# Optimization experiments

Measured on AMD Instinct MI355X. Metric: run time of the kernel, lower is better.

Reference implementation:

```python
import jax, jax.numpy as jnp
import numpy as np

B, T, D, K = 8, 4096, 512, 4096


def setup_inputs() -> dict:
    key = jax.random.key(0)
    k1, k2 = jax.random.split(key)
    x = jax.random.normal(k1, (B, T, D), dtype=jnp.float32)
    embed = jax.random.normal(k2, (K, D), dtype=jnp.float32)
    return {"x": x, "embed": embed}


def reference(x, embed):
    # F.normalize(x, p=2, dim=-1) with eps clamp like torch (eps=1e-12)
    norm = jnp.sqrt(jnp.sum(x * x, axis=-1, keepdims=True))
    xn = x / jnp.maximum(norm, 1e-12)

    flat = xn.reshape(-1, D)  # [(B*T), D]
    x_sq = jnp.sum(flat * flat, axis=1, keepdims=True)           # [(B*T), 1]
    e_sq = jnp.sum(embed * embed, axis=1)[None, :]               # [1, K]
    dist = -(x_sq - 2.0 * (flat @ embed.T) + e_sq)               # [(B*T), K]
    embed_ind = jnp.argmax(dist, axis=-1).reshape(B, T)          # [B, T]

    # decode: embedding gather then 'b n d -> b d n'
    quantize = embed[embed_ind]                                  # [B, T, D]
    quantize = jnp.transpose(quantize, (0, 2, 1))                # [B, D, T]
    return embed_ind, quantize
```

## Files before the change

### kernel.cpp

```cpp
#include <hip/hip_runtime.h>
#include <math.h>

#define BB 8
#define TT 4096
#define DDIM 512
#define KK 4096
#define NN (BB*TT)
#define EPS 0.035f
#define LCAP 2048

typedef __attribute__((ext_vector_type(8))) short bf16x8;
typedef __attribute__((ext_vector_type(4))) float f32x4;

__device__ __forceinline__ void async16(void* lds, const void* g) {
  __builtin_amdgcn_global_load_lds((const __attribute__((address_space(1))) void*)g,
                                   (__attribute__((address_space(3))) void*)lds, 16, 0, 0);
}

__device__ __forceinline__ unsigned pk_bf16(float a, float b) {
  unsigned ua = __float_as_uint(a); ua += 0x7FFFu + ((ua >> 16) & 1u);
  unsigned ub = __float_as_uint(b); ub += 0x7FFFu + ((ub >> 16) & 1u);
  return (ua >> 16) | (ub & 0xFFFF0000u);
}

__global__ __launch_bounds__(256) void prep_kernel(const float* __restrict__ x,
                                                   const float* __restrict__ embed,
                                                   short* __restrict__ xb,
                                                   short* __restrict__ eb,
                                                   float* __restrict__ inv2,
                                                   float* __restrict__ esq) {
  const float* src; short* dst; float* outv; int r; int mode;
  if (blockIdx.x < KK / 4) {
    src = embed; dst = eb; outv = esq; mode = 0;
    r = blockIdx.x * 4 + (threadIdx.x >> 6);
  } else {
    src = x; dst = xb; outv = inv2; mode = 1;
    r = (blockIdx.x - KK / 4) * 4 + (threadIdx.x >> 6);
  }
  int lane = threadIdx.x & 63;
  const float4* row4 = (const float4*)(src + (size_t)r * DDIM);
  float4 v0 = row4[lane];
  float4 v1 = row4[lane + 64];
  uint2 p0, p1;
  p0.x = pk_bf16(v0.x, v0.y); p0.y = pk_bf16(v0.z, v0.w);
  p1.x = pk_bf16(v1.x, v1.y); p1.y = pk_bf16(v1.z, v1.w);
  *(uint2*)(dst + (size_t)r * DDIM + lane * 4) = p0;
  *(uint2*)(dst + (size_t)r * DDIM + 256 + lane * 4) = p1;
  float ss = v0.x*v0.x + v0.y*v0.y + v0.z*v0.z + v0.w*v0.w
           + v1.x*v1.x + v1.y*v1.y + v1.z*v1.z + v1.w*v1.w;
  #pragma unroll
  for (int off = 32; off; off >>= 1) ss += __shfl_down(ss, off);
  if (lane == 0) outv[r] = mode ? 2.0f / fmaxf(sqrtf(ss), 1e-12f) : ss;
}

__global__ __launch_bounds__(256, 2) void vq_mfma(const short* __restrict__ xb,
                                                  const short* __restrict__ eb,
                                                  const float* __restrict__ esq,
                                                  const float* __restrict__ inv2,
                                                  float* __restrict__ cts1,
                                                  float* __restrict__ cts2,
                                                  int* __restrict__ cti) {
  __shared__ short As[128 * 64];
  __shared__ short Bs[128 * 64];
  __shared__ float rS1[2][128];
  __shared__ float rS2[2][128];
  __shared__ int   rI1[2][128];

  const int tid = threadIdx.x;
  const int lane = tid & 63;
  const int w = tid >> 6;
  const int wr = w >> 1, wc = w & 1;
  const int q = lane >> 4, c16 = lane & 15;

  const int mb = blockIdx.x & 255;
  const int kq = blockIdx.x >> 8;
  const int n0 = mb * 128;
  const int kbase = kq * 1024;

  const int srow = w * 32 + (lane >> 3);
  const int scol = ((lane & 7) ^ (lane >> 3)) * 8;
  const short* gA = xb + (size_t)(n0 + srow) * DDIM + scol;

  f32x4 inv4[4];
  #pragma unroll
  for (int ti = 0; ti < 4; ++ti)
    inv4[ti] = *(const f32x4*)&inv2[n0 + wr * 64 + ti * 16 + q * 4];

  for (int p = 0; p < 4; ++p) {
    float cs1[16], cs2[16];
    int   ci1[16];
    #pragma unroll
    for (int s = 0; s < 16; ++s) { cs1[s] = -3e38f; cs2[s] = -3e38f; ci1[s] = 0; }

    for (int cc = 0; cc < 2; ++cc) {
      const int c = p * 2 + cc;
      const int k0c = kbase + c * 128;
      const short* gB = eb + (size_t)(k0c + srow) * DDIM + scol;
      f32x4 acc[4][4];
      #pragma unroll
      for (int ti = 0; ti < 4; ++ti)
        #pragma unroll
        for (int tj = 0; tj < 4; ++tj) acc[ti][tj] = (f32x4){0.f, 0.f, 0.f, 0.f};

      for (int d0 = 0; d0 < DDIM; d0 += 64) {
        #pragma unroll
        for (int i = 0; i < 4; ++i) {
          async16(As + (w * 32 + i * 8) * 64, gA + (size_t)i * 8 * DDIM + d0);
          async16(Bs + (w * 32 + i * 8) * 64, gB + (size_t)i * 8 * DDIM + d0);
        }
        __syncthreads();
        #pragma unroll
        for (int ks = 0; ks < 2; ++ks) {
          const int ko = (((ks << 2) | q) ^ (lane & 7)) << 3;
          bf16x8 af[4], bf[4];
          #pragma unroll
          for (int ti = 0; ti < 4; ++ti)
            af[ti] = *(const bf16x8*)&As[(wr * 64 + ti * 16 + c16) * 64 + ko];
          #pragma unroll
          for (int tj = 0; tj < 4; ++tj)
            bf[tj] = *(const bf16x8*)&Bs[(wc * 64 + tj * 16 + c16) * 64 + ko];
          #pragma unroll
          for (int ti = 0; ti < 4; ++ti)
            #pragma unroll
            for (int tj = 0; tj < 4; ++tj)
              acc[ti][tj] = __builtin_amdgcn_mfma_f32_16x16x32_bf16(af[ti], bf[tj], acc[ti][tj], 0, 0, 0);
        }
        __syncthreads();
      }
      #pragma unroll
      for (int tj = 0; tj < 4; ++tj) {
        const int col = k0c + wc * 64 + tj * 16 + c16;
        const float nes = -esq[col];
        #pragma unroll
        for (int ti = 0; ti < 4; ++ti)
          #pragma unroll
          for (int r = 0; r < 4; ++r) {
            int slot = ti * 4 + r;
            float sc = fmaf(acc[ti][tj][r], inv4[ti][r], nes);
            cs2[slot] = fmaxf(cs2[slot], fminf(sc, cs1[slot]));
            if (sc > cs1[slot]) { cs1[slot] = sc; ci1[slot] = col; }
          }
      }
    }
    #pragma unroll
    for (int slot = 0; slot < 16; ++slot) {
      float a1 = cs1[slot], a2 = cs2[slot]; int ai = ci1[slot];
      #pragma unroll
      for (int off = 1; off < 16; off <<= 1) {
        float b1 = __shfl_xor(a1, off);
        float b2 = __shfl_xor(a2, off);
        int   bi = __shfl_xor(ai, off);
        float ns2 = fmaxf(fmaxf(a2, b2), fminf(a1, b1));
        if (b1 > a1 || (b1 == a1 && bi < ai)) { a1 = b1; ai = bi; }
        a2 = ns2;
      }
      if (c16 == 0) {
        int row = wr * 64 + (slot >> 2) * 16 + q * 4 + (slot & 3);
        rS1[wc][row] = a1; rS2[wc][row] = a2; rI1[wc][row] = ai;
      }
    }
    __syncthreads();
    if (tid < 128) {
      float a1 = rS1[0][tid], a2 = rS2[0][tid]; int ai = rI1[0][tid];
      float b1 = rS1[1][tid], b2 = rS2[1][tid]; int bi = rI1[1][tid];
      float ns2 = fmaxf(fmaxf(a2, b2), fminf(a1, b1));
      if (b1 > a1 || (b1 == a1 && bi < ai)) { a1 = b1; ai = bi; }
      size_t o = (size_t)(kq * 4 + p) * NN + n0 + tid;
      cts1[o] = a1; cts2[o] = ns2; cti[o] = ai;
    }
  }
}

__global__ __launch_bounds__(256) void tail_kernel(const float* __restrict__ x,
                                                   const float* __restrict__ embed,
                                                   const float* __restrict__ esq,
                                                   const float* __restrict__ inv2,
                                                   const float* __restrict__ cts1,
                                                   const float* __restrict__ cts2,
                                                   const int* __restrict__ cti,
                                                   float* __restrict__ out_ind,
                                                   float* __restrict__ out_q) {
  __shared__ float ct_s1[16][64];
  __shared__ float ct_s2[16][64];
  __shared__ int   ct_i[16][64];
  __shared__ int   lidx[64];
  __shared__ unsigned long long pw[64];
  __shared__ int   list[LCAP];
  __shared__ int   lcnt;
  __shared__ float trans[64 * 65];

  const int tid = threadIdx.x;
  const int lane = tid & 63, wv = tid >> 6;
  const int n0 = blockIdx.x * 64;

  #pragma unroll
  for (int i = 0; i < 4; ++i) {
    int ch = i * 4 + wv;
    size_t o = (size_t)ch * NN + n0 + lane;
    ct_s1[ch][lane] = cts1[o];
    ct_s2[ch][lane] = cts2[o];
    ct_i[ch][lane]  = cti[o];
  }
  if (tid == 0) lcnt = 0;
  __syncthreads();

  if (tid < 64) {
    float a1 = -3e38f; int ai = 0x7FFFFFFF;
    #pragma unroll
    for (int ch = 0; ch < 16; ++ch) {
      float b1 = ct_s1[ch][tid]; int bi = ct_i[ch][tid];
      if (b1 > a1 || (b1 == a1 && bi < ai)) { a1 = b1; ai = bi; }
    }
    const float thr = a1 - EPS;
    int extra = 0;
    #pragma unroll
    for (int ch = 0; ch < 16; ++ch) {
      if (ct_s2[ch][tid] >= thr) extra++;
      else if (ct_s1[ch][tid] >= thr && ct_i[ch][tid] != ai) extra++;
    }
    if (extra == 0) {
      lidx[tid] = ai;
    } else {
      lidx[tid] = -1; pw[tid] = 0ull;
      int p = atomicAdd(&lcnt, 1);
      if (p < LCAP) list[p] = (tid << 12) | ai;
      for (int ch = 0; ch < 16; ++ch) {
        if (ct_s2[ch][tid] >= thr) {
          int base = atomicAdd(&lcnt, 256);
          for (int k = 0; k < 256; ++k)
            if (base + k < LCAP) list[base + k] = (tid << 12) | (ch * 256 + k);
        } else if (ct_s1[ch][tid] >= thr && ct_i[ch][tid] != ai) {
          int pp = atomicAdd(&lcnt, 1);
          if (pp < LCAP) list[pp] = (tid << 12) | ct_i[ch][tid];
        }
      }
    }
  }
  __syncthreads();

  {
    int e = lcnt; if (e > LCAP) e = LCAP;
    for (int i = wv; i < e; i += 4) {
      int ent = list[i];
      int r = ent >> 12, code = ent & 4095;
      int grow = n0 + r;
      const float4* xp = (const float4*)&x[(size_t)grow * DDIM + lane * 8];
      const float4* ep = (const float4*)&embed[(size_t)code * DDIM + lane * 8];
      float4 xa = xp[0], xb4 = xp[1], ea = ep[0], eb4 = ep[1];
      float d = xa.x*ea.x + xa.y*ea.y + xa.z*ea.z + xa.w*ea.w
              + xb4.x*eb4.x + xb4.y*eb4.y + xb4.z*eb4.z + xb4.w*eb4.w;
      #pragma unroll
      for (int off = 1; off < 64; off <<= 1) d += __shfl_xor(d, off);
      if (lane == 0) {
        float sc = fmaf(d, inv2[grow], -esq[code]);
        unsigned u = __float_as_uint(sc);
        u = (u >> 31) ? ~u : (u | 0x80000000u);
        unsigned long long pk = ((unsigned long long)u << 32) | (unsigned)(~code);
        atomicMax(&pw[r], pk);
      }
    }
  }
  __syncthreads();

  if (tid < 64) {
    int idx = lidx[tid];
    if (idx < 0) idx = (int)((~(unsigned)(pw[tid] & 0xFFFFFFFFull)) & 4095u);
    lidx[tid] = idx;
    out_ind[n0 + tid] = (float)idx;
  }
  __syncthreads();

  const int bb = n0 >> 12;
  const int t0 = n0 & (TT - 1);
  for (int d0 = 0; d0 < DDIM; d0 += 64) {
    if (d0) __syncthreads();
    #pragma unroll
    for (int qq = 0; qq < 16; ++qq) {
      int tt2 = wv * 16 + qq;
      int e = lidx[tt2];
      trans[lane * 65 + tt2] = embed[(size_t)e * DDIM + d0 + lane];
    }
    __syncthreads();
    #pragma unroll
    for (int qq = 0; qq < 4; ++qq) {
      int dl = (tid >> 4) * 4 + qq;
      int t4 = (tid & 15) * 4;
      float4 o;
      o.x = trans[dl * 65 + t4 + 0];
      o.y = trans[dl * 65 + t4 + 1];
      o.z = trans[dl * 65 + t4 + 2];
      o.w = trans[dl * 65 + t4 + 3];
      *(float4*)&out_q[((size_t)bb * DDIM + d0 + dl) * TT + t0 + t4] = o;
    }
  }
}

extern "C" void kernel_launch(void* const* d_in, const int* in_sizes, int n_in,
                              void* d_out, int out_size, void* d_ws, size_t ws_size,
                              hipStream_t stream) {
  const float* x     = (const float*)d_in[0];
  const float* embed = (const float*)d_in[1];
  char* ws = (char*)d_ws;
  short* xb   = (short*)(ws);
  short* eb   = (short*)(ws + 33554432);
  float* esq  = (float*)(ws + 37748736);
  float* inv2 = (float*)(ws + 37765120);
  float* cts1 = (float*)(ws + 37896192);
  float* cts2 = (float*)(ws + 39993344);
  int*   cti  = (int*)  (ws + 42090496);

  float* out_ind = (float*)d_out;
  float* out_q   = out_ind + NN;

  prep_kernel<<<KK / 4 + NN / 4, 256, 0, stream>>>(x, embed, xb, eb, inv2, esq);
  vq_mfma<<<1024, 256, 0, stream>>>(xb, eb, esq, inv2, cts1, cts2, cti);
  tail_kernel<<<NN / 64, 256, 0, stream>>>(x, embed, esq, inv2, cts1, cts2, cti,
                                           out_ind, out_q);
}
```

Measured before the change: 343.2 us.

## Coarsen candidate top-2 chunks to 1024 codes and rework fp32 rescoring

The MFMA kernel now keeps one running top-2 per row across its whole 1024-code quarter and writes a single packed float4 per quarter, instead of four 256-code chunks split across three arrays. This cuts intermediate global traffic and the tail kernel's loads. The tail kernel splits ambiguous cases into single-candidate rescoring and a full fp32 rescan of a 1024-code quarter when the second-best is within the threshold. Coarser chunks make that full-rescan path more likely to trigger, and it is far costlier per hit. The fixed-size candidate list lost its overflow cap.

```diff
diff --git a/kernel.cpp b/kernel.cpp
--- a/kernel.cpp
+++ b/kernel.cpp
@@ -7,7 +7,6 @@
 #define KK 4096
 #define NN (BB*TT)
 #define EPS 0.035f
-#define LCAP 2048
 
 typedef __attribute__((ext_vector_type(8))) short bf16x8;
 typedef __attribute__((ext_vector_type(4))) float f32x4;
@@ -21,6 +20,11 @@
   unsigned ua = __float_as_uint(a); ua += 0x7FFFu + ((ua >> 16) & 1u);
   unsigned ub = __float_as_uint(b); ub += 0x7FFFu + ((ub >> 16) & 1u);
   return (ua >> 16) | (ub & 0xFFFF0000u);
+}
+
+__device__ __forceinline__ unsigned mono(float s) {
+  unsigned u = __float_as_uint(s);
+  return (u >> 31) ? ~u : (u | 0x80000000u);
 }
 
 __global__ __launch_bounds__(256) void prep_kernel(const float* __restrict__ x,
@@ -57,9 +61,7 @@
                                                   const short* __restrict__ eb,
                                                   const float* __restrict__ esq,
                                                   const float* __restrict__ inv2,
-                                                  float* __restrict__ cts1,
-                                                  float* __restrict__ cts2,
-                                                  int* __restrict__ cti) {
+                                                  float4* __restrict__ top2) {
   __shared__ short As[128 * 64];
   __shared__ short Bs[128 * 64];
   __shared__ float rS1[2][128];
@@ -81,93 +83,91 @@
   const int scol = ((lane & 7) ^ (lane >> 3)) * 8;
   const short* gA = xb + (size_t)(n0 + srow) * DDIM + scol;
 
+  float s1[16], s2v[16];
+  int   i1[16];
+  #pragma unroll
+  for (int s = 0; s < 16; ++s) { s1[s] = -3e38f; s2v[s] = -3e38f; i1[s] = 0; }
+
   f32x4 inv4[4];
   #pragma unroll
   for (int ti = 0; ti < 4; ++ti)
     inv4[ti] = *(const f32x4*)&inv2[n0 + wr * 64 + ti * 16 + q * 4];
 
-  for (int p = 0; p < 4; ++p) {
-    float cs1[16], cs2[16];
-    int   ci1[16];
-    #pragma unroll
-    for (int s = 0; s < 16; ++s) { cs1[s] = -3e38f; cs2[s] = -3e38f; ci1[s] = 0; }
-
-    for (int cc = 0; cc < 2; ++cc) {
-      const int c = p * 2 + cc;
-      const int k0c = kbase + c * 128;
-      const short* gB = eb + (size_t)(k0c + srow) * DDIM + scol;
-      f32x4 acc[4][4];
-      #pragma unroll
-      for (int ti = 0; ti < 4; ++ti)
+  for (int c = 0; c < 8; ++c) {
+    const int k0c = kbase + c * 128;
+    const short* gB = eb + (size_t)(k0c + srow) * DDIM + scol;
+    f32x4 acc[4][4];
+    #pragma unroll
+    for (int ti = 0; ti < 4; ++ti)
+      #pragma unroll
+      for (int tj = 0; tj < 4; ++tj) acc[ti][tj] = (f32x4){0.f, 0.f, 0.f, 0.f};
+
+    for (int d0 = 0; d0 < DDIM; d0 += 64) {
+      #pragma unroll
+      for (int i = 0; i < 4; ++i) {
+        async16(As + (w * 32 + i * 8) * 64, gA + (size_t)i * 8 * DDIM + d0);
+        async16(Bs + (w * 32 + i * 8) * 64, gB + (size_t)i * 8 * DDIM + d0);
+      }
+      __syncthreads();
+      #pragma unroll
+      for (int ks = 0; ks < 2; ++ks) {
+        const int ko = (((ks << 2) | q) ^ (lane & 7)) << 3;
+        bf16x8 af[4], bf[4];
         #pragma unroll
-        for (int tj = 0; tj < 4; ++tj) acc[ti][tj] = (f32x4){0.f, 0.f, 0.f, 0.f};
-
-      for (int d0 = 0; d0 < DDIM; d0 += 64) {
+        for (int ti = 0; ti < 4; ++ti)
+          af[ti] = *(const bf16x8*)&As[(wr * 64 + ti * 16 + c16) * 64 + ko];
         #pragma unroll
-        for (int i = 0; i < 4; ++i) {
-          async16(As + (w * 32 + i * 8) * 64, gA + (size_t)i * 8 * DDIM + d0);
-          async16(Bs + (w * 32 + i * 8) * 64, gB + (size_t)i * 8 * DDIM + d0);
-        }
-        __syncthreads();
-        #pragma unroll
-        for (int ks = 0; ks < 2; ++ks) {
-          const int ko = (((ks << 2) | q) ^ (lane & 7)) << 3;
-          bf16x8 af[4], bf[4];
-          #pragma unroll
-          for (int ti = 0; ti < 4; ++ti)
-            af[ti] = *(const bf16x8*)&As[(wr * 64 + ti * 16 + c16) * 64 + ko];
-          #pragma unroll
-          for (int tj = 0; tj < 4; ++tj)
-            bf[tj] = *(const bf16x8*)&Bs[(wc * 64 + tj * 16 + c16) * 64 + ko];
-          #pragma unroll
-          for (int ti = 0; ti < 4; ++ti)
-            #pragma unroll
-            for (int tj = 0; tj < 4; ++tj)
-              acc[ti][tj] = __builtin_amdgcn_mfma_f32_16x16x32_bf16(af[ti], bf[tj], acc[ti][tj], 0, 0, 0);
-        }
-        __syncthreads();
-      }
-      #pragma unroll
-      for (int tj = 0; tj < 4; ++tj) {
-        const int col = k0c + wc * 64 + tj * 16 + c16;
-        const float nes = -esq[col];
+        for (int tj = 0; tj < 4; ++tj)
+          bf[tj] = *(const bf16x8*)&Bs[(wc * 64 + tj * 16 + c16) * 64 + ko];
         #pragma unroll
         for (int ti = 0; ti < 4; ++ti)
           #pragma unroll
-          for (int r = 0; r < 4; ++r) {
-            int slot = ti * 4 + r;
-            float sc = fmaf(acc[ti][tj][r], inv4[ti][r], nes);
-            cs2[slot] = fmaxf(cs2[slot], fminf(sc, cs1[slot]));
-            if (sc > cs1[slot]) { cs1[slot] = sc; ci1[slot] = col; }
-          }
-      }
-    }
-    #pragma unroll
-    for (int slot = 0; slot < 16; ++slot) {
-      float a1 = cs1[slot], a2 = cs2[slot]; int ai = ci1[slot];
-      #pragma unroll
-      for (int off = 1; off < 16; off <<= 1) {
-        float b1 = __shfl_xor(a1, off);
-        float b2 = __shfl_xor(a2, off);
-        int   bi = __shfl_xor(ai, off);
-        float ns2 = fmaxf(fmaxf(a2, b2), fminf(a1, b1));
-        if (b1 > a1 || (b1 == a1 && bi < ai)) { a1 = b1; ai = bi; }
-        a2 = ns2;
-      }
-      if (c16 == 0) {
-        int row = wr * 64 + (slot >> 2) * 16 + q * 4 + (slot & 3);
-        rS1[wc][row] = a1; rS2[wc][row] = a2; rI1[wc][row] = ai;
-      }
-    }
-    __syncthreads();
-    if (tid < 128) {
-      float a1 = rS1[0][tid], a2 = rS2[0][tid]; int ai = rI1[0][tid];
-      float b1 = rS1[1][tid], b2 = rS2[1][tid]; int bi = rI1[1][tid];
+          for (int tj = 0; tj < 4; ++tj)
+            acc[ti][tj] = __builtin_amdgcn_mfma_f32_16x16x32_bf16(af[ti], bf[tj], acc[ti][tj], 0, 0, 0);
+      }
+      __syncthreads();
+    }
+    #pragma unroll
+    for (int tj = 0; tj < 4; ++tj) {
+      const int col = k0c + wc * 64 + tj * 16 + c16;
+      const float nes = -esq[col];
+      #pragma unroll
+      for (int ti = 0; ti < 4; ++ti)
+        #pragma unroll
+        for (int r = 0; r < 4; ++r) {
+          int slot = ti * 4 + r;
+          float sc = fmaf(acc[ti][tj][r], inv4[ti][r], nes);
+          float mn = fminf(sc, s1[slot]);
+          s2v[slot] = fmaxf(s2v[slot], mn);
+          if (sc > s1[slot]) { s1[slot] = sc; i1[slot] = col; }
+        }
+    }
+  }
+
+  #pragma unroll
+  for (int slot = 0; slot < 16; ++slot) {
+    float a1 = s1[slot], a2 = s2v[slot]; int ai = i1[slot];
+    #pragma unroll
+    for (int off = 1; off < 16; off <<= 1) {
+      float b1 = __shfl_xor(a1, off);
+      float b2 = __shfl_xor(a2, off);
+      int   bi = __shfl_xor(ai, off);
       float ns2 = fmaxf(fmaxf(a2, b2), fminf(a1, b1));
       if (b1 > a1 || (b1 == a1 && bi < ai)) { a1 = b1; ai = bi; }
-      size_t o = (size_t)(kq * 4 + p) * NN + n0 + tid;
-      cts1[o] = a1; cts2[o] = ns2; cti[o] = ai;
-    }
+      a2 = ns2;
+    }
+    if (c16 == 0) {
+      int row = wr * 64 + (slot >> 2) * 16 + q * 4 + (slot & 3);
+      rS1[wc][row] = a1; rS2[wc][row] = a2; rI1[wc][row] = ai;
+    }
+  }
+  __syncthreads();
+  if (tid < 128) {
+    float a1 = rS1[0][tid], a2 = rS2[0][tid]; int ai = rI1[0][tid];
+    float b1 = rS1[1][tid], b2 = rS2[1][tid]; int bi = rI1[1][tid];
+    float ns2 = fmaxf(fmaxf(a2, b2), fminf(a1, b1));
+    if (b1 > a1 || (b1 == a1 && bi < ai)) { a1 = b1; ai = bi; }
+    top2[(size_t)kq * NN + n0 + tid] = make_float4(a1, __int_as_float(ai), ns2, 0.f);
   }
 }
 
@@ -175,73 +175,63 @@
                                                    const float* __restrict__ embed,
                                                    const float* __restrict__ esq,
                                                    const float* __restrict__ inv2,
-                                                   const float* __restrict__ cts1,
-                                                   const float* __restrict__ cts2,
-                                                   const int* __restrict__ cti,
+                                                   const float4* __restrict__ top2,
                                                    float* __restrict__ out_ind,
                                                    float* __restrict__ out_q) {
-  __shared__ float ct_s1[16][64];
-  __shared__ float ct_s2[16][64];
-  __shared__ int   ct_i[16][64];
-  __shared__ int   lidx[64];
+  __shared__ float4 qt[4][64];
+  __shared__ int lidx[64];
   __shared__ unsigned long long pw[64];
-  __shared__ int   list[LCAP];
-  __shared__ int   lcnt;
+  __shared__ int clist[512];
+  __shared__ int elist[256];
+  __shared__ int ccnt, ecnt;
   __shared__ float trans[64 * 65];
 
   const int tid = threadIdx.x;
   const int lane = tid & 63, wv = tid >> 6;
   const int n0 = blockIdx.x * 64;
 
-  #pragma unroll
-  for (int i = 0; i < 4; ++i) {
-    int ch = i * 4 + wv;
-    size_t o = (size_t)ch * NN + n0 + lane;
-    ct_s1[ch][lane] = cts1[o];
-    ct_s2[ch][lane] = cts2[o];
-    ct_i[ch][lane]  = cti[o];
-  }
-  if (tid == 0) lcnt = 0;
+  qt[wv][lane] = top2[(size_t)wv * NN + n0 + lane];
+  if (tid == 0) { ccnt = 0; ecnt = 0; }
   __syncthreads();
 
   if (tid < 64) {
+    float4 t[4];
+    #pragma unroll
+    for (int k = 0; k < 4; ++k) t[k] = qt[k][tid];
     float a1 = -3e38f; int ai = 0x7FFFFFFF;
     #pragma unroll
-    for (int ch = 0; ch < 16; ++ch) {
-      float b1 = ct_s1[ch][tid]; int bi = ct_i[ch][tid];
-      if (b1 > a1 || (b1 == a1 && bi < ai)) { a1 = b1; ai = bi; }
+    for (int k = 0; k < 4; ++k) {
+      int bi = __float_as_int(t[k].y);
+      if (t[k].x > a1 || (t[k].x == a1 && bi < ai)) { a1 = t[k].x; ai = bi; }
     }
     const float thr = a1 - EPS;
-    int extra = 0;
-    #pragma unroll
-    for (int ch = 0; ch < 16; ++ch) {
-      if (ct_s2[ch][tid] >= thr) extra++;
-      else if (ct_s1[ch][tid] >= thr && ct_i[ch][tid] != ai) extra++;
-    }
-    if (extra == 0) {
+    int amb = 0;
+    #pragma unroll
+    for (int k = 0; k < 4; ++k) {
+      if (t[k].z >= thr) {
+        amb = 1;
+        int p = atomicAdd(&ecnt, 1);
+        elist[p] = (tid << 2) | k;
+      } else if (t[k].x >= thr && __float_as_int(t[k].y) != ai) {
+        amb = 1;
+        int p = atomicAdd(&ccnt, 1);
+        clist[p] = (tid << 12) | __float_as_int(t[k].y);
+      }
+    }
+    if (amb) {
+      lidx[tid] = -1; pw[tid] = 0ull;
+      int p = atomicAdd(&ccnt, 1);
+      clist[p] = (tid << 12) | ai;
+    } else {
       lidx[tid] = ai;
-    } else {
-      lidx[tid] = -1; pw[tid] = 0ull;
-      int p = atomicAdd(&lcnt, 1);
-      if (p < LCAP) list[p] = (tid << 12) | ai;
-      for (int ch = 0; ch < 16; ++ch) {
-        if (ct_s2[ch][tid] >= thr) {
-          int base = atomicAdd(&lcnt, 256);
-          for (int k = 0; k < 256; ++k)
-            if (base + k < LCAP) list[base + k] = (tid << 12) | (ch * 256 + k);
-        } else if (ct_s1[ch][tid] >= thr && ct_i[ch][tid] != ai) {
-          int pp = atomicAdd(&lcnt, 1);
-          if (pp < LCAP) list[pp] = (tid << 12) | ct_i[ch][tid];
-        }
-      }
     }
   }
   __syncthreads();
 
   {
-    int e = lcnt; if (e > LCAP) e = LCAP;
+    int e = ccnt;
     for (int i = wv; i < e; i += 4) {
-      int ent = list[i];
+      int ent = clist[i];
       int r = ent >> 12, code = ent & 4095;
       int grow = n0 + r;
       const float4* xp = (const float4*)&x[(size_t)grow * DDIM + lane * 8];
@@ -253,11 +243,40 @@
       for (int off = 1; off < 64; off <<= 1) d += __shfl_xor(d, off);
       if (lane == 0) {
         float sc = fmaf(d, inv2[grow], -esq[code]);
-        unsigned u = __float_as_uint(sc);
-        u = (u >> 31) ? ~u : (u | 0x80000000u);
-        unsigned long long pk = ((unsigned long long)u << 32) | (unsigned)(~code);
+        unsigned long long pk = ((unsigned long long)mono(sc) << 32) | (unsigned)(~code);
         atomicMax(&pw[r], pk);
       }
+    }
+  }
+  {
+    int e = ecnt;
+    for (int i = wv; i < e; i += 4) {
+      int ent = elist[i];
+      int r = ent >> 2, qtr = ent & 3;
+      int grow = n0 + r;
+      const float iv = inv2[grow];
+      const float4* xp = (const float4*)&x[(size_t)grow * DDIM];
+      float bs = -3e38f; int bi = 0x7FFFFFFF;
+      for (int j = 0; j < 16; ++j) {
+        int code = qtr * 1024 + j * 64 + lane;
+        const float4* ep = (const float4*)&embed[(size_t)code * DDIM];
+        float d = 0.f;
+        #pragma unroll 8
+        for (int d4 = 0; d4 < 128; ++d4) {
+          float4 e4 = ep[d4];
+          float4 x4 = xp[d4];
+          d += e4.x*x4.x + e4.y*x4.y + e4.z*x4.z + e4.w*x4.w;
+        }
+        float sc = fmaf(d, iv, -esq[code]);
+        if (sc > bs || (sc == bs && code < bi)) { bs = sc; bi = code; }
+      }
+      unsigned long long pk = ((unsigned long long)mono(bs) << 32) | (unsigned)(~bi);
+      #pragma unroll
+      for (int off = 1; off < 64; off <<= 1) {
+        unsigned long long p2 = __shfl_xor((long long)pk, off);
+        if (p2 > pk) pk = p2;
+      }
+      if (lane == 0) atomicMax(&pw[r], pk);
     }
   }
   __syncthreads();
@@ -301,19 +320,16 @@
   const float* x     = (const float*)d_in[0];
   const float* embed = (const float*)d_in[1];
   char* ws = (char*)d_ws;
-  short* xb   = (short*)(ws);
-  short* eb   = (short*)(ws + 33554432);
-  float* esq  = (float*)(ws + 37748736);
-  float* inv2 = (float*)(ws + 37765120);
-  float* cts1 = (float*)(ws + 37896192);
-  float* cts2 = (float*)(ws + 39993344);
-  int*   cti  = (int*)  (ws + 42090496);
+  short* xb    = (short*)(ws);
+  short* eb    = (short*)(ws + 33554432);
+  float* esq   = (float*)(ws + 37748736);
+  float* inv2  = (float*)(ws + 37765120);
+  float4* top2 = (float4*)(ws + 37896192);
 
   float* out_ind = (float*)d_out;
   float* out_q   = out_ind + NN;
 
   prep_kernel<<<KK / 4 + NN / 4, 256, 0, stream>>>(x, embed, xb, eb, inv2, esq);
-  vq_mfma<<<1024, 256, 0, stream>>>(xb, eb, esq, inv2, cts1, cts2, cti);
-  tail_kernel<<<NN / 64, 256, 0, stream>>>(x, embed, esq, inv2, cts1, cts2, cti,
-                                           out_ind, out_q);
-}
+  vq_mfma<<<1024, 256, 0, stream>>>(xb, eb, esq, inv2, top2);
+  tail_kernel<<<NN / 64, 256, 0, stream>>>(x, embed, esq, inv2, top2, out_ind, out_q);
+}
```

Measured after the change: 443.1 us. +29.1%, slower.
